# Kernel optimization log

Measured on AMD Instinct MI355X. Metric: run time of the kernel, lower is better.

Reference implementation:

```python
import jax, jax.numpy as jnp
import numpy as np

B, L, D, H = 8, 256, 256, 8
DH = D // H
NEG = jnp.float32(-(2 ** 32) + 1)


def _split_heads(x):
    # [B, L, D] -> [H, B, L, DH]  (tf.split axis=2 + concat axis=0 stacks heads slowest)
    b, l, d = x.shape
    return x.reshape(b, l, H, DH).transpose(2, 0, 1, 3)


def _split_heads_t(t):
    # [B, L, L, D] -> [H, B, L, L, DH]
    b, q, k, d = t.shape
    return t.reshape(b, q, k, H, DH).transpose(3, 0, 1, 2, 4)


def setup_inputs() -> dict:
    key = jax.random.key(0)
    ks = jax.random.split(key, 12)
    s = 1.0 / np.sqrt(D)
    return {
        "queries": jax.random.normal(ks[0], (B, L, D), jnp.float32),
        "keys": jax.random.normal(ks[1], (B, L, D), jnp.float32),
        "time_matrix_K": jax.random.normal(ks[2], (B, L, L, D), jnp.float32),
        "time_matrix_V": jax.random.normal(ks[3], (B, L, L, D), jnp.float32),
        "absolute_pos_K": jax.random.normal(ks[4], (B, L, D), jnp.float32),
        "absolute_pos_V": jax.random.normal(ks[5], (B, L, D), jnp.float32),
        "Wq": jax.random.normal(ks[6], (D, D), jnp.float32) * s,
        "bq": jnp.zeros((D,), jnp.float32),
        "Wk": jax.random.normal(ks[7], (D, D), jnp.float32) * s,
        "bk": jnp.zeros((D,), jnp.float32),
        "Wv": jax.random.normal(ks[8], (D, D), jnp.float32) * s,
        "bv": jnp.zeros((D,), jnp.float32),
    }


def reference(queries, keys, time_matrix_K, time_matrix_V,
              absolute_pos_K, absolute_pos_V, Wq, bq, Wk, bk, Wv, bv):
    Qh = _split_heads(queries @ Wq + bq)          # [H,B,L,DH]
    Kh = _split_heads(keys @ Wk + bk)
    Vh = _split_heads(keys @ Wv + bv)
    Pk = _split_heads(absolute_pos_K)
    Pv = _split_heads(absolute_pos_V)
    Tk = _split_heads_t(time_matrix_K)            # [H,B,L,L,DH]
    Tv = _split_heads_t(time_matrix_V)

    scores = (jnp.einsum('hbqd,hbkd->hbqk', Qh, Kh)
              + jnp.einsum('hbqd,hbkd->hbqk', Qh, Pk)
              + jnp.einsum('hbqkd,hbqd->hbqk', Tk, Qh))
    scores = scores / jnp.float32(np.sqrt(DH))

    # key padding mask: rows of `keys` summing to exactly 0 are padding
    key_mask = jnp.sign(jnp.abs(jnp.sum(keys, axis=-1)))   # [B,L]
    scores = jnp.where(key_mask[None, :, None, :] == 0, NEG, scores)
    # causal mask
    tril = jnp.tril(jnp.ones((L, L), jnp.float32))
    scores = jnp.where(tril[None, None, :, :] == 0, NEG, scores)

    attn = jax.nn.softmax(scores, axis=-1)                  # [H,B,L,L]
    query_mask = jnp.sign(jnp.abs(jnp.sum(queries, axis=-1)))  # [B,L]
    attn = attn * query_mask[None, :, :, None]
    # dropout is identity at inference (dropout_rate=0)

    out = (jnp.einsum('hbqk,hbkd->hbqd', attn, Vh)
           + jnp.einsum('hbqk,hbkd->hbqd', attn, Pv)
           + jnp.einsum('hbqk,hbqkd->hbqd', attn, Tv))      # [H,B,L,DH]

    out = out.transpose(1, 2, 0, 3).reshape(B, L, D)        # concat heads
    return out + queries
```

## Files before the change

### kernel.cpp

```cpp
#include <hip/hip_runtime.h>

#define L 256
#define D 256
#define H 8
#define DH 32

static constexpr float NEGV = -4294967296.0f;
static constexpr float INV_SQRT_DH = 0.17677669529663687f;

__global__ __launch_bounds__(256) void proj3_kernel(
    const float* __restrict__ queries, const float* __restrict__ keys,
    const float* __restrict__ Wq, const float* __restrict__ bq,
    const float* __restrict__ Wk, const float* __restrict__ bk,
    const float* __restrict__ Wv, const float* __restrict__ bv,
    const float* __restrict__ pk, const float* __restrict__ pv,
    float* __restrict__ Qo, float* __restrict__ KPko, float* __restrict__ VPvo)
{
    __shared__ float As[16][68];
    __shared__ float Bs[16][64];

    const float* A; const float* W; const float* bias; const float* add; float* out;
    if (blockIdx.z == 0)      { A = queries; W = Wq; bias = bq; add = nullptr; out = Qo; }
    else if (blockIdx.z == 1) { A = keys;    W = Wk; bias = bk; add = pk;      out = KPko; }
    else                      { A = keys;    W = Wv; bias = bv; add = pv;      out = VPvo; }

    const int t  = threadIdx.x;
    const int bm = blockIdx.x * 64;
    const int bn = blockIdx.y * 64;

    const int ar = t >> 2;
    const int ak = (t & 3) << 2;
    const int br = t >> 4;
    const int bc = (t & 15) << 2;
    const int tm = (t >> 4) << 2;
    const int tn = (t & 15) << 2;

    float acc[4][4] = {};

    for (int k0 = 0; k0 < 256; k0 += 16) {
        const float4 a4 = *(const float4*)&A[(bm + ar) * 256 + k0 + ak];
        const float4 b4 = *(const float4*)&W[(k0 + br) * 256 + bn + bc];
        As[ak + 0][ar] = a4.x; As[ak + 1][ar] = a4.y;
        As[ak + 2][ar] = a4.z; As[ak + 3][ar] = a4.w;
        *(float4*)&Bs[br][bc] = b4;
        __syncthreads();

        #pragma unroll
        for (int kk = 0; kk < 16; ++kk) {
            const float4 a = *(const float4*)&As[kk][tm];
            const float4 bb = *(const float4*)&Bs[kk][tn];
            const float aa[4] = {a.x, a.y, a.z, a.w};
            const float bbv[4] = {bb.x, bb.y, bb.z, bb.w};
            #pragma unroll
            for (int i = 0; i < 4; ++i)
                #pragma unroll
                for (int jj = 0; jj < 4; ++jj)
                    acc[i][jj] = fmaf(aa[i], bbv[jj], acc[i][jj]);
        }
        __syncthreads();
    }

    const float4 bias4 = *(const float4*)&bias[bn + tn];
    #pragma unroll
    for (int i = 0; i < 4; ++i) {
        const int row = bm + tm + i;
        float4 o;
        o.x = acc[i][0] + bias4.x; o.y = acc[i][1] + bias4.y;
        o.z = acc[i][2] + bias4.z; o.w = acc[i][3] + bias4.w;
        if (add) {
            const float4 a4 = *(const float4*)&add[row * 256 + bn + tn];
            o.x += a4.x; o.y += a4.y; o.z += a4.z; o.w += a4.w;
        }
        *(float4*)&out[row * 256 + bn + tn] = o;
    }
}

__global__ __launch_bounds__(256) void mask_kernel(
    const float* __restrict__ keys, const float* __restrict__ queries,
    float* __restrict__ kmask, float* __restrict__ qmask)
{
    const int wid  = (blockIdx.x * 256 + threadIdx.x) >> 6;
    const int lane = threadIdx.x & 63;
    const float* src = (wid < 2048) ? keys : queries;
    const int row = (wid < 2048) ? wid : (wid - 2048);

    const float4 v = *(const float4*)&src[row * 256 + (lane << 2)];
    float s = v.x + v.y + v.z + v.w;
    #pragma unroll
    for (int o = 1; o < 64; o <<= 1) s += __shfl_xor(s, o);
    if (lane == 0) {
        const float m = (s != 0.0f) ? 1.0f : 0.0f;
        if (wid < 2048) kmask[row] = m; else qmask[row] = m;
    }
}

#define LP (L + 4)

__global__ __launch_bounds__(256) void attn_kernel(
    const float* __restrict__ Qm, const float* __restrict__ KPk,
    const float* __restrict__ VPv, const float* __restrict__ Tk,
    const float* __restrict__ Tv, const float* __restrict__ kmask,
    const float* __restrict__ qmask, const float* __restrict__ queries,
    float* __restrict__ out)
{
    const int bid = blockIdx.x;
    const int b   = bid >> 8;
    const int j0  = bid & 255;
    const int q   = (b & 1) ? (255 - j0) : j0;
    const int bq  = (b << 8) + q;
    const int t  = threadIdx.x;
    const int w    = t >> 6;
    const int lane = t & 63;

    __shared__ float qrow[D];
    __shared__ float kmrow[L];
    __shared__ float sc[H][LP];
    __shared__ int   allneg[H];
    __shared__ float4 red[256];

    qrow[t]  = Qm[bq * D + t];
    kmrow[t] = kmask[(b << 8) + t];
    #pragma unroll
    for (int i = t; i < H * LP; i += 256) (&sc[0][0])[i] = NEGV;
    __syncthreads();

    const int hB = lane >> 3;
    const int jB = lane & 7;
    const size_t tbase = (size_t)bq << 16;
    const float4 qv = *(const float4*)&qrow[lane << 2];

    #pragma unroll 2
    for (int k = w; k <= q; k += 4) {
        const float4 kv  = *(const float4*)&KPk[((b << 8) + k) * 256 + (lane << 2)];
        const float4 tkv = *(const float4*)&Tk[tbase + ((size_t)k << 8) + (lane << 2)];
        float p = qv.x * (kv.x + tkv.x);
        p = fmaf(qv.y, kv.y + tkv.y, p);
        p = fmaf(qv.z, kv.z + tkv.z, p);
        p = fmaf(qv.w, kv.w + tkv.w, p);
        p += __shfl_xor(p, 1);
        p += __shfl_xor(p, 2);
        p += __shfl_xor(p, 4);
        if (jB == 0)
            sc[hB][k] = (kmrow[k] != 0.0f) ? p * INV_SQRT_DH : NEGV;
    }
    __syncthreads();

    #pragma unroll
    for (int hh = 0; hh < 2; ++hh) {
        const int h = (w << 1) + hh;
        float v0 = sc[h][lane];
        float v1 = sc[h][lane + 64];
        float v2 = sc[h][lane + 128];
        float v3 = sc[h][lane + 192];
        float m = fmaxf(fmaxf(v0, v1), fmaxf(v2, v3));
        #pragma unroll
        for (int o = 1; o < 64; o <<= 1) m = fmaxf(m, __shfl_xor(m, o));
        const float e0 = __expf(v0 - m), e1 = __expf(v1 - m);
        const float e2 = __expf(v2 - m), e3 = __expf(v3 - m);
        float s = e0 + e1 + e2 + e3;
        #pragma unroll
        for (int o = 1; o < 64; o <<= 1) s += __shfl_xor(s, o);
        const float r = 1.0f / s;
        sc[h][lane]       = e0 * r;
        sc[h][lane + 64]  = e1 * r;
        sc[h][lane + 128] = e2 * r;
        sc[h][lane + 192] = e3 * r;
        if (lane == 0) allneg[h] = (m == NEGV) ? 1 : 0;
    }
    __syncthreads();

    const int dg = lane;
    const int h  = dg >> 3;
    const int kmax = allneg[h] ? L : (q + 1);

    float4 acc = make_float4(0.f, 0.f, 0.f, 0.f);
    #pragma unroll 2
    for (int k = w; k < kmax; k += 4) {
        const float a = sc[h][k];
        const float4 v   = *(const float4*)&VPv[((b << 8) + k) * 256 + (dg << 2)];
        const float4 tvv = *(const float4*)&Tv[tbase + ((size_t)k << 8) + (dg << 2)];
        acc.x = fmaf(a, v.x + tvv.x, acc.x);
        acc.y = fmaf(a, v.y + tvv.y, acc.y);
        acc.z = fmaf(a, v.z + tvv.z, acc.z);
        acc.w = fmaf(a, v.w + tvv.w, acc.w);
    }
    red[t] = acc;
    __syncthreads();

    if (t < 64) {
        const float4 r0 = red[t], r1 = red[t + 64], r2 = red[t + 128], r3 = red[t + 192];
        const float qmv = qmask[bq];
        const float4 qv2 = *(const float4*)&queries[bq * 256 + (t << 2)];
        float4 o;
        o.x = (r0.x + r1.x + r2.x + r3.x) * qmv + qv2.x;
        o.y = (r0.y + r1.y + r2.y + r3.y) * qmv + qv2.y;
        o.z = (r0.z + r1.z + r2.z + r3.z) * qmv + qv2.z;
        o.w = (r0.w + r1.w + r2.w + r3.w) * qmv + qv2.w;
        *(float4*)&out[bq * 256 + (t << 2)] = o;
    }
}

extern "C" void kernel_launch(void* const* d_in, const int* in_sizes, int n_in,
                              void* d_out, int out_size, void* d_ws, size_t ws_size,
                              hipStream_t stream)
{
    const float* queries = (const float*)d_in[0];
    const float* keys    = (const float*)d_in[1];
    const float* Tk      = (const float*)d_in[2];
    const float* Tv      = (const float*)d_in[3];
    const float* pk      = (const float*)d_in[4];
    const float* pv      = (const float*)d_in[5];
    const float* Wq      = (const float*)d_in[6];
    const float* bq      = (const float*)d_in[7];
    const float* Wk      = (const float*)d_in[8];
    const float* bk      = (const float*)d_in[9];
    const float* Wv      = (const float*)d_in[10];
    const float* bv      = (const float*)d_in[11];
    float* out = (float*)d_out;

    float* ws  = (float*)d_ws;
    float* Q   = ws;
    float* KPk = ws + 524288;
    float* VPv = ws + 1048576;
    float* km  = ws + 1572864;
    float* qm  = ws + 1574912;

    dim3 pgrid(2048 / 64, 256 / 64, 3);
    proj3_kernel<<<pgrid, 256, 0, stream>>>(queries, keys, Wq, bq, Wk, bk,
                                            Wv, bv, pk, pv, Q, KPk, VPv);
    mask_kernel<<<1024, 256, 0, stream>>>(keys, queries, km, qm);
    attn_kernel<<<2048, 256, 0, stream>>>(Q, KPk, VPv, Tk, Tv, km, qm, queries, out);
}
```

Measured before the change: 146.2 us.

## Use contiguous per-wave key ranges with software prefetch in attention kernel

Each wave now handles a contiguous chunk of key rows instead of striding by 4, and both the score and value loops load the next row before computing on the current one. This double-buffers the global loads and gives each wave a sequential stream through Tk/Tv. The change also rotates the query-row mapping per batch pair to spread heavy causal rows across the grid, and sets a launch-bounds occupancy hint of 8 blocks. The cost is more register pressure from the prefetch and a separate fallback loop for fully masked rows.

```diff
diff --git a/kernel.cpp b/kernel.cpp
--- a/kernel.cpp
+++ b/kernel.cpp
@@ -96,7 +96,7 @@
 
 #define LP (L + 4)
 
-__global__ __launch_bounds__(256) void attn_kernel(
+__global__ __launch_bounds__(256, 8) void attn_kernel(
     const float* __restrict__ Qm, const float* __restrict__ KPk,
     const float* __restrict__ VPv, const float* __restrict__ Tk,
     const float* __restrict__ Tv, const float* __restrict__ kmask,
@@ -106,9 +106,10 @@
     const int bid = blockIdx.x;
     const int b   = bid >> 8;
     const int j0  = bid & 255;
-    const int q   = (b & 1) ? (255 - j0) : j0;
+    const int jr  = (j0 + ((b >> 1) << 6)) & 255;
+    const int q   = (b & 1) ? (255 - jr) : jr;
     const int bq  = (b << 8) + q;
-    const int t  = threadIdx.x;
+    const int t    = threadIdx.x;
     const int w    = t >> 6;
     const int lane = t & 63;
 
@@ -124,24 +125,39 @@
     for (int i = t; i < H * LP; i += 256) (&sc[0][0])[i] = NEGV;
     __syncthreads();
 
-    const int hB = lane >> 3;
-    const int jB = lane & 7;
+    const int rows = q + 1;
+    const int base = rows >> 2;
+    const int rem  = rows & 3;
+    const int lo   = w * base + (w < rem ? w : rem);
+    const int cnt  = base + (w < rem ? 1 : 0);
+    const int hi   = lo + cnt;
+
     const size_t tbase = (size_t)bq << 16;
-    const float4 qv = *(const float4*)&qrow[lane << 2];
-
-    #pragma unroll 2
-    for (int k = w; k <= q; k += 4) {
-        const float4 kv  = *(const float4*)&KPk[((b << 8) + k) * 256 + (lane << 2)];
-        const float4 tkv = *(const float4*)&Tk[tbase + ((size_t)k << 8) + (lane << 2)];
-        float p = qv.x * (kv.x + tkv.x);
-        p = fmaf(qv.y, kv.y + tkv.y, p);
-        p = fmaf(qv.z, kv.z + tkv.z, p);
-        p = fmaf(qv.w, kv.w + tkv.w, p);
-        p += __shfl_xor(p, 1);
-        p += __shfl_xor(p, 2);
-        p += __shfl_xor(p, 4);
-        if (jB == 0)
-            sc[hB][k] = (kmrow[k] != 0.0f) ? p * INV_SQRT_DH : NEGV;
+
+    {
+        const int hB = lane >> 3;
+        const int jB = lane & 7;
+        const float4 qv = *(const float4*)&qrow[lane << 2];
+        const float4* kp = (const float4*)&KPk[((b << 8) + lo) * 256 + (lane << 2)];
+        const float4* tp = (const float4*)&Tk[tbase + ((size_t)lo << 8) + (lane << 2)];
+        if (cnt > 0) {
+            float4 kv = *kp, tkv = *tp;
+            for (int k = lo; k < hi; ++k) {
+                const int adv = (k + 1 < hi) ? 64 : 0;
+                kp += adv; tp += adv;
+                const float4 kvn = *kp, tkvn = *tp;
+                float p = qv.x * (kv.x + tkv.x);
+                p = fmaf(qv.y, kv.y + tkv.y, p);
+                p = fmaf(qv.z, kv.z + tkv.z, p);
+                p = fmaf(qv.w, kv.w + tkv.w, p);
+                p += __shfl_xor(p, 1);
+                p += __shfl_xor(p, 2);
+                p += __shfl_xor(p, 4);
+                if (jB == 0)
+                    sc[hB][k] = (kmrow[k] != 0.0f) ? p * INV_SQRT_DH : NEGV;
+                kv = kvn; tkv = tkvn;
+            }
+        }
     }
     __syncthreads();
 
@@ -171,18 +187,36 @@
 
     const int dg = lane;
     const int h  = dg >> 3;
-    const int kmax = allneg[h] ? L : (q + 1);
 
     float4 acc = make_float4(0.f, 0.f, 0.f, 0.f);
-    #pragma unroll 2
-    for (int k = w; k < kmax; k += 4) {
-        const float a = sc[h][k];
-        const float4 v   = *(const float4*)&VPv[((b << 8) + k) * 256 + (dg << 2)];
-        const float4 tvv = *(const float4*)&Tv[tbase + ((size_t)k << 8) + (dg << 2)];
-        acc.x = fmaf(a, v.x + tvv.x, acc.x);
-        acc.y = fmaf(a, v.y + tvv.y, acc.y);
-        acc.z = fmaf(a, v.z + tvv.z, acc.z);
-        acc.w = fmaf(a, v.w + tvv.w, acc.w);
+    {
+        const float4* vp = (const float4*)&VPv[((b << 8) + lo) * 256 + (dg << 2)];
+        const float4* tp = (const float4*)&Tv[tbase + ((size_t)lo << 8) + (dg << 2)];
+        if (cnt > 0) {
+            float4 vv = *vp, tvv = *tp;
+            for (int k = lo; k < hi; ++k) {
+                const int adv = (k + 1 < hi) ? 64 : 0;
+                vp += adv; tp += adv;
+                const float4 vn = *vp, tvn = *tp;
+                const float a = sc[h][k];
+                acc.x = fmaf(a, vv.x + tvv.x, acc.x);
+                acc.y = fmaf(a, vv.y + tvv.y, acc.y);
+                acc.z = fmaf(a, vv.z + tvv.z, acc.z);
+                acc.w = fmaf(a, vv.w + tvv.w, acc.w);
+                vv = vn; tvv = tvn;
+            }
+        }
+    }
+    if (allneg[h]) {
+        for (int k = q + 1 + w; k < L; k += 4) {
+            const float a = sc[h][k];
+            const float4 vv  = *(const float4*)&VPv[((b << 8) + k) * 256 + (dg << 2)];
+            const float4 tvv = *(const float4*)&Tv[tbase + ((size_t)k << 8) + (dg << 2)];
+            acc.x = fmaf(a, vv.x + tvv.x, acc.x);
+            acc.y = fmaf(a, vv.y + tvv.y, acc.y);
+            acc.z = fmaf(a, vv.z + tvv.z, acc.z);
+            acc.w = fmaf(a, vv.w + tvv.w, acc.w);
+        }
     }
     red[t] = acc;
     __syncthreads();
```

Result: slower. 152.7 us (+4.4%).

## Split fused attention into score, softmax, chunked PV and reduce kernels

Applied to the files above, without the earlier changes.

Replaces the single per-query attention kernel with four kernels. Scores are computed in 64-key chunks across 8192 blocks and written to a workspace score buffer, softmax runs as its own pass, the PV product is again split into key chunks producing partial sums, and a final kernel reduces them and applies the query mask and residual. This spreads the causally imbalanced work over more blocks to improve load balance and parallelism. The cost is extra launches and round trips of the score and partial buffers through global memory. The old path remains as a fallback when the workspace is too small.

```diff
diff --git a/kernel.cpp b/kernel.cpp
--- a/kernel.cpp
+++ b/kernel.cpp
@@ -92,6 +92,175 @@
         const float m = (s != 0.0f) ? 1.0f : 0.0f;
         if (wid < 2048) kmask[row] = m; else qmask[row] = m;
     }
+}
+
+__global__ __launch_bounds__(256) void score_kernel(
+    const float* __restrict__ Qm, const float* __restrict__ KPk,
+    const float* __restrict__ Tk, float* __restrict__ sc)
+{
+    const int bid = blockIdx.x;
+    const int tt  = bid >> 11;
+    const int bj  = bid & 2047;
+    const int b   = bj >> 8;
+    const int j   = bj & 255;
+    const int q   = (b & 1) ? (255 - j) : j;
+    const int bq  = (b << 8) + q;
+
+    const int lo = tt << 6;
+    if (lo > q) return;
+    const int hi = (lo + 64 < q + 1) ? lo + 64 : q + 1;
+
+    const int t = threadIdx.x;
+    const int w = t >> 6, lane = t & 63;
+    const int hB = lane >> 3, jB = lane & 7;
+
+    const float4 qv = *(const float4*)&Qm[bq * 256 + (lane << 2)];
+    const size_t tbase = (size_t)bq << 16;
+    float* scout = sc + ((size_t)bq << 11);
+
+    #pragma unroll 2
+    for (int k = lo + w; k < hi; k += 4) {
+        const float4 kv  = *(const float4*)&KPk[((b << 8) + k) * 256 + (lane << 2)];
+        const float4 tkv = *(const float4*)&Tk[tbase + ((size_t)k << 8) + (lane << 2)];
+        float p = qv.x * (kv.x + tkv.x);
+        p = fmaf(qv.y, kv.y + tkv.y, p);
+        p = fmaf(qv.z, kv.z + tkv.z, p);
+        p = fmaf(qv.w, kv.w + tkv.w, p);
+        p += __shfl_xor(p, 1);
+        p += __shfl_xor(p, 2);
+        p += __shfl_xor(p, 4);
+        if (jB == 0) scout[(hB << 8) + k] = p;
+    }
+}
+
+__global__ __launch_bounds__(256) void softmax_kernel(
+    float* __restrict__ sc, const float* __restrict__ kmask,
+    int* __restrict__ allneg_ws)
+{
+    const int bq = blockIdx.x;
+    const int b  = bq >> 8;
+    const int q  = bq & 255;
+    const int t  = threadIdx.x;
+    const int w = t >> 6, lane = t & 63;
+
+    __shared__ float kmrow[L];
+    kmrow[t] = kmask[(b << 8) + t];
+    __syncthreads();
+
+    #pragma unroll
+    for (int hh = 0; hh < 2; ++hh) {
+        const int h = (w << 1) + hh;
+        float* row = sc + ((size_t)bq << 11) + (h << 8);
+        float v[4];
+        #pragma unroll
+        for (int i = 0; i < 4; ++i) {
+            const int k = lane + (i << 6);
+            const float raw = row[k];
+            v[i] = (k <= q && kmrow[k] != 0.0f) ? raw * INV_SQRT_DH : NEGV;
+        }
+        float m = fmaxf(fmaxf(v[0], v[1]), fmaxf(v[2], v[3]));
+        #pragma unroll
+        for (int o = 1; o < 64; o <<= 1) m = fmaxf(m, __shfl_xor(m, o));
+        float e[4], s = 0.f;
+        #pragma unroll
+        for (int i = 0; i < 4; ++i) { e[i] = __expf(v[i] - m); s += e[i]; }
+        #pragma unroll
+        for (int o = 1; o < 64; o <<= 1) s += __shfl_xor(s, o);
+        const float r = 1.0f / s;
+        #pragma unroll
+        for (int i = 0; i < 4; ++i) row[lane + (i << 6)] = e[i] * r;
+        if (h == 0 && lane == 0) allneg_ws[bq] = (m == NEGV) ? 1 : 0;
+    }
+}
+
+__global__ __launch_bounds__(256) void outp_kernel(
+    const float* __restrict__ prob, const float* __restrict__ VPv,
+    const float* __restrict__ Tv, const int* __restrict__ allneg_ws,
+    float* __restrict__ partial)
+{
+    const int bid = blockIdx.x;
+    const int tt  = bid >> 11;
+    const int bj  = bid & 2047;
+    const int b   = bj >> 8;
+    const int j   = bj & 255;
+    const int q   = (b & 1) ? (255 - j) : j;
+    const int bq  = (b << 8) + q;
+
+    const int t = threadIdx.x;
+    const int w = t >> 6, lane = t & 63;
+    const int lo = tt << 6;
+    const int an = allneg_ws[bq];
+    const int hi = an ? (lo + 64) : ((lo + 64 < q + 1) ? lo + 64 : q + 1);
+
+    float* slot = partial + ((((size_t)bq << 2) + tt) << 8);
+
+    if (lo >= hi) {
+        if (t < 64)
+            *(float4*)&slot[t << 2] = make_float4(0.f, 0.f, 0.f, 0.f);
+        return;
+    }
+
+    __shared__ float pl[H][68];
+    __shared__ float4 red[256];
+
+    {
+        int idx = t;
+        #pragma unroll
+        for (int r = 0; r < 2; ++r, idx += 256) {
+            const int h = idx >> 6, kk = idx & 63;
+            pl[h][kk] = prob[((size_t)bq << 11) + (h << 8) + lo + kk];
+        }
+    }
+    __syncthreads();
+
+    const int dg = lane;
+    const int h  = dg >> 3;
+    const size_t tbase = (size_t)bq << 16;
+
+    float4 acc = make_float4(0.f, 0.f, 0.f, 0.f);
+    #pragma unroll 2
+    for (int k = lo + w; k < hi; k += 4) {
+        const float a = pl[h][k - lo];
+        const float4 vv  = *(const float4*)&VPv[((b << 8) + k) * 256 + (dg << 2)];
+        const float4 tvv = *(const float4*)&Tv[tbase + ((size_t)k << 8) + (dg << 2)];
+        acc.x = fmaf(a, vv.x + tvv.x, acc.x);
+        acc.y = fmaf(a, vv.y + tvv.y, acc.y);
+        acc.z = fmaf(a, vv.z + tvv.z, acc.z);
+        acc.w = fmaf(a, vv.w + tvv.w, acc.w);
+    }
+    red[t] = acc;
+    __syncthreads();
+
+    if (t < 64) {
+        const float4 r0 = red[t], r1 = red[t + 64], r2 = red[t + 128], r3 = red[t + 192];
+        float4 o;
+        o.x = r0.x + r1.x + r2.x + r3.x;
+        o.y = r0.y + r1.y + r2.y + r3.y;
+        o.z = r0.z + r1.z + r2.z + r3.z;
+        o.w = r0.w + r1.w + r2.w + r3.w;
+        *(float4*)&slot[t << 2] = o;
+    }
+}
+
+__global__ __launch_bounds__(64) void reduce_kernel(
+    const float* __restrict__ partial, const float* __restrict__ qmask,
+    const float* __restrict__ queries, float* __restrict__ out)
+{
+    const int bq = blockIdx.x;
+    const int t  = threadIdx.x;
+    const float* base = partial + (((size_t)bq << 2) << 8) + (t << 2);
+    const float4 p0 = *(const float4*)(base);
+    const float4 p1 = *(const float4*)(base + 256);
+    const float4 p2 = *(const float4*)(base + 512);
+    const float4 p3 = *(const float4*)(base + 768);
+    const float qmv = qmask[bq];
+    const float4 qv = *(const float4*)&queries[bq * 256 + (t << 2)];
+    float4 o;
+    o.x = (p0.x + p1.x + p2.x + p3.x) * qmv + qv.x;
+    o.y = (p0.y + p1.y + p2.y + p3.y) * qmv + qv.y;
+    o.z = (p0.z + p1.z + p2.z + p3.z) * qmv + qv.z;
+    o.w = (p0.w + p1.w + p2.w + p3.w) * qmv + qv.w;
+    *(float4*)&out[bq * 256 + (t << 2)] = o;
 }
 
 #define LP (L + 4)
@@ -219,15 +388,27 @@
     float* out = (float*)d_out;
 
     float* ws  = (float*)d_ws;
-    float* Q   = ws;
-    float* KPk = ws + 524288;
-    float* VPv = ws + 1048576;
-    float* km  = ws + 1572864;
-    float* qm  = ws + 1574912;
+    float* Q    = ws;
+    float* KPk  = ws + 524288;
+    float* VPv  = ws + 1048576;
+    float* km   = ws + 1572864;
+    float* qm   = ws + 1574912;
+    float* sc   = ws + 1576960;
+    float* part = ws + 5771264;
+    int*   anf  = (int*)(ws + 7868416);
+    const size_t REQ = (size_t)(7868416 + 2048) * 4;
 
     dim3 pgrid(2048 / 64, 256 / 64, 3);
     proj3_kernel<<<pgrid, 256, 0, stream>>>(queries, keys, Wq, bq, Wk, bk,
                                             Wv, bv, pk, pv, Q, KPk, VPv);
     mask_kernel<<<1024, 256, 0, stream>>>(keys, queries, km, qm);
-    attn_kernel<<<2048, 256, 0, stream>>>(Q, KPk, VPv, Tk, Tv, km, qm, queries, out);
-}
+
+    if (ws_size >= REQ) {
+        score_kernel<<<8192, 256, 0, stream>>>(Q, KPk, Tk, sc);
+        softmax_kernel<<<2048, 256, 0, stream>>>(sc, km, anf);
+        outp_kernel<<<8192, 256, 0, stream>>>(sc, VPv, Tv, anf, part);
+        reduce_kernel<<<2048, 64, 0, stream>>>(part, qm, queries, out);
+    } else {
+        attn_kernel<<<2048, 256, 0, stream>>>(Q, KPk, VPv, Tk, Tv, km, qm, queries, out);
+    }
+}
```

New measurement: 183.1 us. 1.25x slower.

## Pair causal query rows per block with 512 threads for balanced attention work

Applied to the files above, without the earlier changes.

Each attention block now handles two query rows, q and 255-q, in sequence with 8 waves instead of 4. This makes the causal work per block uniform, where before each block's work grew with its query index. The grid is halved. It adds an extra pass of barriers and serializes the two rows inside one block, and the larger blocks may reduce occupancy.

```diff
diff --git a/kernel.cpp b/kernel.cpp
--- a/kernel.cpp
+++ b/kernel.cpp
@@ -96,7 +96,7 @@
 
 #define LP (L + 4)
 
-__global__ __launch_bounds__(256) void attn_kernel(
+__global__ __launch_bounds__(512) void attn_pair_kernel(
     const float* __restrict__ Qm, const float* __restrict__ KPk,
     const float* __restrict__ VPv, const float* __restrict__ Tk,
     const float* __restrict__ Tv, const float* __restrict__ kmask,
@@ -104,11 +104,9 @@
     float* __restrict__ out)
 {
     const int bid = blockIdx.x;
-    const int b   = bid >> 8;
-    const int j0  = bid & 255;
-    const int q   = (b & 1) ? (255 - j0) : j0;
-    const int bq  = (b << 8) + q;
-    const int t  = threadIdx.x;
+    const int b   = bid >> 7;
+    const int j   = bid & 127;
+    const int t    = threadIdx.x;
     const int w    = t >> 6;
     const int lane = t & 63;
 
@@ -116,87 +114,100 @@
     __shared__ float kmrow[L];
     __shared__ float sc[H][LP];
     __shared__ int   allneg[H];
-    __shared__ float4 red[256];
-
-    qrow[t]  = Qm[bq * D + t];
-    kmrow[t] = kmask[(b << 8) + t];
+    __shared__ float4 red[512];
+
+    if (t < 256) kmrow[t] = kmask[(b << 8) + t];
+
     #pragma unroll
-    for (int i = t; i < H * LP; i += 256) (&sc[0][0])[i] = NEGV;
-    __syncthreads();
-
-    const int hB = lane >> 3;
-    const int jB = lane & 7;
-    const size_t tbase = (size_t)bq << 16;
-    const float4 qv = *(const float4*)&qrow[lane << 2];
-
-    #pragma unroll 2
-    for (int k = w; k <= q; k += 4) {
-        const float4 kv  = *(const float4*)&KPk[((b << 8) + k) * 256 + (lane << 2)];
-        const float4 tkv = *(const float4*)&Tk[tbase + ((size_t)k << 8) + (lane << 2)];
-        float p = qv.x * (kv.x + tkv.x);
-        p = fmaf(qv.y, kv.y + tkv.y, p);
-        p = fmaf(qv.z, kv.z + tkv.z, p);
-        p = fmaf(qv.w, kv.w + tkv.w, p);
-        p += __shfl_xor(p, 1);
-        p += __shfl_xor(p, 2);
-        p += __shfl_xor(p, 4);
-        if (jB == 0)
-            sc[hB][k] = (kmrow[k] != 0.0f) ? p * INV_SQRT_DH : NEGV;
-    }
-    __syncthreads();
-
-    #pragma unroll
-    for (int hh = 0; hh < 2; ++hh) {
-        const int h = (w << 1) + hh;
-        float v0 = sc[h][lane];
-        float v1 = sc[h][lane + 64];
-        float v2 = sc[h][lane + 128];
-        float v3 = sc[h][lane + 192];
-        float m = fmaxf(fmaxf(v0, v1), fmaxf(v2, v3));
-        #pragma unroll
-        for (int o = 1; o < 64; o <<= 1) m = fmaxf(m, __shfl_xor(m, o));
-        const float e0 = __expf(v0 - m), e1 = __expf(v1 - m);
-        const float e2 = __expf(v2 - m), e3 = __expf(v3 - m);
-        float s = e0 + e1 + e2 + e3;
-        #pragma unroll
-        for (int o = 1; o < 64; o <<= 1) s += __shfl_xor(s, o);
-        const float r = 1.0f / s;
-        sc[h][lane]       = e0 * r;
-        sc[h][lane + 64]  = e1 * r;
-        sc[h][lane + 128] = e2 * r;
-        sc[h][lane + 192] = e3 * r;
-        if (lane == 0) allneg[h] = (m == NEGV) ? 1 : 0;
-    }
-    __syncthreads();
-
-    const int dg = lane;
-    const int h  = dg >> 3;
-    const int kmax = allneg[h] ? L : (q + 1);
-
-    float4 acc = make_float4(0.f, 0.f, 0.f, 0.f);
-    #pragma unroll 2
-    for (int k = w; k < kmax; k += 4) {
-        const float a = sc[h][k];
-        const float4 v   = *(const float4*)&VPv[((b << 8) + k) * 256 + (dg << 2)];
-        const float4 tvv = *(const float4*)&Tv[tbase + ((size_t)k << 8) + (dg << 2)];
-        acc.x = fmaf(a, v.x + tvv.x, acc.x);
-        acc.y = fmaf(a, v.y + tvv.y, acc.y);
-        acc.z = fmaf(a, v.z + tvv.z, acc.z);
-        acc.w = fmaf(a, v.w + tvv.w, acc.w);
-    }
-    red[t] = acc;
-    __syncthreads();
-
-    if (t < 64) {
-        const float4 r0 = red[t], r1 = red[t + 64], r2 = red[t + 128], r3 = red[t + 192];
-        const float qmv = qmask[bq];
-        const float4 qv2 = *(const float4*)&queries[bq * 256 + (t << 2)];
-        float4 o;
-        o.x = (r0.x + r1.x + r2.x + r3.x) * qmv + qv2.x;
-        o.y = (r0.y + r1.y + r2.y + r3.y) * qmv + qv2.y;
-        o.z = (r0.z + r1.z + r2.z + r3.z) * qmv + qv2.z;
-        o.w = (r0.w + r1.w + r2.w + r3.w) * qmv + qv2.w;
-        *(float4*)&out[bq * 256 + (t << 2)] = o;
+    for (int pass = 0; pass < 2; ++pass) {
+        const int q  = pass ? (255 - j) : j;
+        const int bq = (b << 8) + q;
+        const size_t tbase = (size_t)bq << 16;
+
+        if (t < 256) qrow[t] = Qm[bq * D + t];
+        for (int i = t; i < H * LP; i += 512) (&sc[0][0])[i] = NEGV;
+        __syncthreads();
+
+        {
+            const int hB = lane >> 3;
+            const int jB = lane & 7;
+            const float4 qv = *(const float4*)&qrow[lane << 2];
+            #pragma unroll 2
+            for (int k = w; k <= q; k += 8) {
+                const float4 kv  = *(const float4*)&KPk[((b << 8) + k) * 256 + (lane << 2)];
+                const float4 tkv = *(const float4*)&Tk[tbase + ((size_t)k << 8) + (lane << 2)];
+                float p = qv.x * (kv.x + tkv.x);
+                p = fmaf(qv.y, kv.y + tkv.y, p);
+                p = fmaf(qv.z, kv.z + tkv.z, p);
+                p = fmaf(qv.w, kv.w + tkv.w, p);
+                p += __shfl_xor(p, 1);
+                p += __shfl_xor(p, 2);
+                p += __shfl_xor(p, 4);
+                if (jB == 0)
+                    sc[hB][k] = (kmrow[k] != 0.0f) ? p * INV_SQRT_DH : NEGV;
+            }
+        }
+        __syncthreads();
+
+        {
+            const int h = w;
+            float v0 = sc[h][lane];
+            float v1 = sc[h][lane + 64];
+            float v2 = sc[h][lane + 128];
+            float v3 = sc[h][lane + 192];
+            float m = fmaxf(fmaxf(v0, v1), fmaxf(v2, v3));
+            #pragma unroll
+            for (int o = 1; o < 64; o <<= 1) m = fmaxf(m, __shfl_xor(m, o));
+            const float e0 = __expf(v0 - m), e1 = __expf(v1 - m);
+            const float e2 = __expf(v2 - m), e3 = __expf(v3 - m);
+            float s = e0 + e1 + e2 + e3;
+            #pragma unroll
+            for (int o = 1; o < 64; o <<= 1) s += __shfl_xor(s, o);
+            const float r = 1.0f / s;
+            sc[h][lane]       = e0 * r;
+            sc[h][lane + 64]  = e1 * r;
+            sc[h][lane + 128] = e2 * r;
+            sc[h][lane + 192] = e3 * r;
+            if (lane == 0) allneg[h] = (m == NEGV) ? 1 : 0;
+        }
+        __syncthreads();
+
+        {
+            const int dg = lane;
+            const int h  = dg >> 3;
+            const int kmax = allneg[h] ? L : (q + 1);
+
+            float4 acc = make_float4(0.f, 0.f, 0.f, 0.f);
+            #pragma unroll 2
+            for (int k = w; k < kmax; k += 8) {
+                const float a = sc[h][k];
+                const float4 vv  = *(const float4*)&VPv[((b << 8) + k) * 256 + (dg << 2)];
+                const float4 tvv = *(const float4*)&Tv[tbase + ((size_t)k << 8) + (dg << 2)];
+                acc.x = fmaf(a, vv.x + tvv.x, acc.x);
+                acc.y = fmaf(a, vv.y + tvv.y, acc.y);
+                acc.z = fmaf(a, vv.z + tvv.z, acc.z);
+                acc.w = fmaf(a, vv.w + tvv.w, acc.w);
+            }
+            red[t] = acc;
+        }
+        __syncthreads();
+
+        if (t < 64) {
+            float4 o = make_float4(0.f, 0.f, 0.f, 0.f);
+            #pragma unroll
+            for (int i = 0; i < 8; ++i) {
+                const float4 r4 = red[t + (i << 6)];
+                o.x += r4.x; o.y += r4.y; o.z += r4.z; o.w += r4.w;
+            }
+            const float qmv = qmask[bq];
+            const float4 qv2 = *(const float4*)&queries[bq * 256 + (t << 2)];
+            o.x = o.x * qmv + qv2.x;
+            o.y = o.y * qmv + qv2.y;
+            o.z = o.z * qmv + qv2.z;
+            o.w = o.w * qmv + qv2.w;
+            *(float4*)&out[bq * 256 + (t << 2)] = o;
+        }
+        __syncthreads();
     }
 }
 
@@ -229,5 +240,6 @@
     proj3_kernel<<<pgrid, 256, 0, stream>>>(queries, keys, Wq, bq, Wk, bk,
                                             Wv, bv, pk, pv, Q, KPk, VPv);
     mask_kernel<<<1024, 256, 0, stream>>>(keys, queries, km, qm);
-    attn_kernel<<<2048, 256, 0, stream>>>(Q, KPk, VPv, Tk, Tv, km, qm, queries, out);
-}
+    attn_pair_kernel<<<1024, 512, 0, stream>>>(Q, KPk, VPv, Tk, Tv, km, qm,
+                                               queries, out);
+}
```

Measured after the change: 158.9 us. 8.7% more time.
